# Performance work log

Hardware: AMD Instinct MI355X
Metric: run time of the kernel (lower is better)

The kernel has to match this reference:

```python
import jax, jax.numpy as jnp
import numpy as np

NEG_SLOPE = 0.2  # LeakyReLU slope

N, E, D_IN, D_OUT, H, NBIN = 50000, 500000, 256, 256, 8, 10
DH = D_OUT // H


def setup_inputs() -> dict:
    key = jax.random.key(0)
    ks = jax.random.split(key, 9)
    emb_rel = jax.random.normal(ks[0], (N, D_IN), dtype=jnp.float32)
    head_idxs = jax.random.randint(ks[1], (E,), 0, N, dtype=jnp.int32)
    tail_idxs = jax.random.randint(ks[2], (E,), 0, N, dtype=jnp.int32)
    bins = jax.random.randint(ks[3], (E,), 0, NBIN, dtype=jnp.int32)
    # xavier-normal-ish scaled params (gain for relu)
    attn_proj_w = jax.random.normal(ks[4], (D_OUT, 2 * D_IN), dtype=jnp.float32) * (1.4142 * (2.0 / (2 * D_IN + D_OUT)) ** 0.5)
    attn_proj_b = jnp.zeros((D_OUT,), dtype=jnp.float32)
    attn_bin = jax.random.normal(ks[5], (NBIN, H, 1), dtype=jnp.float32) * 0.3
    attn_vec = jax.random.normal(ks[6], (1, H, DH), dtype=jnp.float32) * (1.4142 * (2.0 / (H + DH)) ** 0.5)
    aggr_proj_w = jax.random.normal(ks[7], (D_OUT, D_IN), dtype=jnp.float32) * (1.4142 * (2.0 / (D_IN + D_OUT)) ** 0.5)
    aggr_proj_b = jnp.zeros((D_OUT,), dtype=jnp.float32)
    return {
        "emb_rel": emb_rel,
        "head_idxs": head_idxs,
        "tail_idxs": tail_idxs,
        "bins": bins,
        "attn_proj_w": attn_proj_w,
        "attn_proj_b": attn_proj_b,
        "attn_bin": attn_bin,
        "attn_vec": attn_vec,
        "aggr_proj_w": aggr_proj_w,
        "aggr_proj_b": aggr_proj_b,
        "num_nodes": N,
    }


def reference(emb_rel, head_idxs, tail_idxs, bins, attn_proj_w, attn_proj_b,
              attn_bin, attn_vec, aggr_proj_w, aggr_proj_b, num_nodes):
    num_head, dim_hid = attn_vec.shape[1], attn_vec.shape[2]
    eh = emb_rel[head_idxs]                      # (E, D_in)
    et = emb_rel[tail_idxs]                      # (E, D_in)
    concat = jnp.concatenate([eh, et], axis=-1)  # (E, 2*D_in)
    proj = (concat @ attn_proj_w.T + attn_proj_b).reshape(-1, num_head, dim_hid)
    lrelu = jnp.where(proj >= 0, proj, NEG_SLOPE * proj)
    # raw attention logits per edge/head: (E, H, 1)
    attn_raw = jnp.sum(lrelu * attn_vec, axis=-1, keepdims=True) + attn_bin[bins]
    # segmented softmax over edges grouped by head node
    seg_max = jax.ops.segment_max(attn_raw, head_idxs, num_segments=num_nodes)
    seg_max = jnp.where(jnp.isfinite(seg_max), seg_max, 0.0)  # empty segments -> 0 (never gathered anyway)
    attn_val = jnp.exp(attn_raw - seg_max[head_idxs])
    attn_sums = jax.ops.segment_sum(attn_val, head_idxs, num_segments=num_nodes)
    beta = attn_val / (attn_sums[head_idxs] + 1e-16)            # (E, H, 1)
    aggr = (et @ aggr_proj_w.T + aggr_proj_b).reshape(-1, num_head, dim_hid)
    out = jax.ops.segment_sum(beta * aggr, head_idxs, num_segments=num_nodes)
    return out.reshape(num_nodes, num_head * dim_hid)
```

## Files before the change

kernel.cpp:

```cpp
#include <hip/hip_runtime.h>
#include <math.h>

#define D_IN 256
#define D_OUT 256
#define NH 8
#define DH 32
#define NBIN 10
#define NEG_SLOPE 0.2f

typedef short short8 __attribute__((ext_vector_type(8)));
typedef float f32x4 __attribute__((ext_vector_type(4)));

__device__ __forceinline__ unsigned short f2bf(float f) {
  unsigned u = __float_as_uint(f);
  unsigned r = u + 0x7fffu + ((u >> 16) & 1u);
  return (unsigned short)(r >> 16);
}
__device__ __forceinline__ float bf2f(unsigned short s) {
  return __uint_as_float((unsigned)s << 16);
}

__global__ void pack_weights_kernel(const float* __restrict__ attn_w,
                                    const float* __restrict__ attn_b,
                                    const float* __restrict__ aggr_w,
                                    const float* __restrict__ aggr_b,
                                    unsigned short* __restrict__ WCbf,
                                    float* __restrict__ biasC) {
  int j = blockIdx.x;
  int k = threadIdx.x;
  float v, b = 0.f;
  if (j < 256) {
    v = attn_w[j * 512 + k];
  } else {
    int idx = j - 256, g = idx >> 3, r = idx & 7;
    if (r < 4) { int c = g * 4 + r;     v = attn_w[c * 512 + 256 + k]; b = attn_b[c]; }
    else       { int c = g * 4 + r - 4; v = aggr_w[c * 256 + k];       b = aggr_b[c]; }
  }
  WCbf[j * 256 + k] = f2bf(v);
  if (k == 0) biasC[j] = b;
}

__global__ void emb2bf_kernel(const float* __restrict__ emb,
                              unsigned short* __restrict__ embbf, long long total) {
  long long i = ((long long)blockIdx.x * blockDim.x + threadIdx.x) * 8;
  if (i >= total) return;
  float4 a = *(const float4*)(emb + i);
  float4 b = *(const float4*)(emb + i + 4);
  short8 o;
  o[0] = (short)f2bf(a.x); o[1] = (short)f2bf(a.y);
  o[2] = (short)f2bf(a.z); o[3] = (short)f2bf(a.w);
  o[4] = (short)f2bf(b.x); o[5] = (short)f2bf(b.y);
  o[6] = (short)f2bf(b.z); o[7] = (short)f2bf(b.w);
  *(short8*)(embbf + i) = o;
}

#define EPAD 36
__global__ __launch_bounds__(256) void gemm_bf16_kernel(
    const unsigned short* __restrict__ Abf,
    const unsigned short* __restrict__ Bbf,
    const float* __restrict__ biasC,
    float* __restrict__ P1, unsigned short* __restrict__ P2A, int N) {
  __shared__ char smem[128 * EPAD * 4];
  unsigned short* As = (unsigned short*)smem;
  unsigned short* Bs = (unsigned short*)(smem + 8192);
  float* Ls = (float*)smem;
  const int tid = threadIdx.x;
  const int row0 = blockIdx.y * 128, col0 = blockIdx.x * 128;
  const int wave = tid >> 6, l = tid & 63;
  const int wm = wave >> 1, wn = wave & 1;
  const int lr = l & 15;
  const int lq = l >> 4;
  const int srow = tid >> 2;
  const int sk = (tid & 3) * 8;
  f32x4 acc[4][4] = {};
  for (int kk = 0; kk < 256; kk += 32) {
    int ar0 = row0 + srow;      if (ar0 >= N) ar0 = N - 1;
    int ar1 = row0 + 64 + srow; if (ar1 >= N) ar1 = N - 1;
    short8 a0 = *(const short8*)(Abf + (size_t)ar0 * 256 + kk + sk);
    short8 a1 = *(const short8*)(Abf + (size_t)ar1 * 256 + kk + sk);
    short8 b0 = *(const short8*)(Bbf + (size_t)(col0 + srow) * 256 + kk + sk);
    short8 b1 = *(const short8*)(Bbf + (size_t)(col0 + 64 + srow) * 256 + kk + sk);
    __syncthreads();
    *(short8*)&As[srow * 32 + sk] = a0;
    *(short8*)&As[(64 + srow) * 32 + sk] = a1;
    *(short8*)&Bs[srow * 32 + sk] = b0;
    *(short8*)&Bs[(64 + srow) * 32 + sk] = b1;
    __syncthreads();
    short8 af[4], bfr[4];
#pragma unroll
    for (int i = 0; i < 4; ++i)
      af[i] = *(const short8*)&As[(wm * 64 + i * 16 + lr) * 32 + lq * 8];
#pragma unroll
    for (int j = 0; j < 4; ++j)
      bfr[j] = *(const short8*)&Bs[(wn * 64 + j * 16 + lr) * 32 + lq * 8];
#pragma unroll
    for (int i = 0; i < 4; ++i)
#pragma unroll
      for (int j = 0; j < 4; ++j)
        acc[i][j] = __builtin_amdgcn_mfma_f32_16x16x32_bf16(af[i], bfr[j], acc[i][j], 0, 0, 0);
  }
  for (int j = 0; j < 4; ++j) {
    __syncthreads();
    const float bias = biasC[col0 + wn * 64 + j * 16 + lr];
#pragma unroll
    for (int i = 0; i < 4; ++i) {
      const int lrow = wm * 64 + i * 16 + lq * 4;
#pragma unroll
      for (int r = 0; r < 4; ++r)
        Ls[(lrow + r) * EPAD + wn * 16 + lr] = acc[i][j][r] + bias;
    }
    __syncthreads();
    if (col0 < 256) {
      const int sub = tid & 7, half = sub >> 2, quad = sub & 3;
#pragma unroll
      for (int s = 0; s < 4; ++s) {
        const int row = (tid >> 3) + s * 32;
        const int grow = row0 + row;
        if (grow < N) {
          float4 v = *(const float4*)&Ls[row * EPAD + half * 16 + quad * 4];
          *(float4*)(P1 + (size_t)grow * 256 + col0 + half * 64 + j * 16 + quad * 4) = v;
        }
      }
    } else {
      const int o = tid & 3, half = o >> 1, part = o & 1;
#pragma unroll
      for (int s = 0; s < 2; ++s) {
        const int row = (tid >> 2) + s * 64;
        const int grow = row0 + row;
        if (grow < N) {
          const float* src = &Ls[row * EPAD + half * 16 + part * 8];
          short8 v;
#pragma unroll
          for (int q = 0; q < 8; ++q) v[q] = (short)f2bf(src[q]);
          *(short8*)(P2A + (size_t)grow * 512 + (col0 - 256) + half * 64 + j * 16 + part * 8) = v;
        }
      }
    }
  }
}

__global__ void count_kernel(const int* __restrict__ head, int* __restrict__ deg, int E) {
  int e = blockIdx.x * blockDim.x + threadIdx.x;
  if (e < E) atomicAdd(&deg[head[e]], 1);
}

__global__ __launch_bounds__(256) void scan_partial_kernel(const int* __restrict__ deg,
                                                           int* __restrict__ row_start,
                                                           int* __restrict__ blocksums, int N) {
  __shared__ int wave_tot[4];
  const int t = threadIdx.x;
  const int base = blockIdx.x * 1024 + t * 4;
  int d0 = 0, d1 = 0, d2 = 0, d3 = 0;
  if (base + 0 < N) d0 = deg[base + 0];
  if (base + 1 < N) d1 = deg[base + 1];
  if (base + 2 < N) d2 = deg[base + 2];
  if (base + 3 < N) d3 = deg[base + 3];
  const int s = d0 + d1 + d2 + d3;
  const int lane = t & 63;
  int v = s;
#pragma unroll
  for (int off = 1; off < 64; off <<= 1) {
    int u = __shfl_up(v, off, 64);
    if (lane >= off) v += u;
  }
  if (lane == 63) wave_tot[t >> 6] = v;
  __syncthreads();
  int woff = 0;
  const int w = t >> 6;
  for (int i = 0; i < 4; ++i)
    if (i < w) woff += wave_tot[i];
  const int excl = v - s + woff;
  if (base + 0 < N) row_start[base + 0] = excl;
  if (base + 1 < N) row_start[base + 1] = excl + d0;
  if (base + 2 < N) row_start[base + 2] = excl + d0 + d1;
  if (base + 3 < N) row_start[base + 3] = excl + d0 + d1 + d2;
  if (t == 255) blocksums[blockIdx.x] = excl + s;
}

__global__ void scan_sums_kernel(int* __restrict__ blocksums, int nb) {
  if (threadIdx.x == 0 && blockIdx.x == 0) {
    int run = 0;
    for (int i = 0; i < nb; ++i) {
      int v = blocksums[i];
      blocksums[i] = run;
      run += v;
    }
  }
}

__global__ void add_offsets_kernel(int* __restrict__ row_start, int* __restrict__ cursor,
                                   const int* __restrict__ blocksums, int N) {
  int i = blockIdx.x * blockDim.x + threadIdx.x;
  if (i < N) {
    int v = row_start[i] + blocksums[i >> 10];
    row_start[i] = v;
    cursor[i] = v;
  }
}

__global__ void scatter_kernel(const int* __restrict__ head, const int* __restrict__ tail,
                               const int* __restrict__ bins, int* __restrict__ cursor,
                               int* __restrict__ packed, int E) {
  int e = blockIdx.x * blockDim.x + threadIdx.x;
  if (e >= E) return;
  int pos = atomicAdd(&cursor[head[e]], 1);
  packed[pos] = (bins[e] << 16) | tail[e];
}

__global__ __launch_bounds__(256) void node_aggr_kernel(
    const float* __restrict__ P1, const unsigned short* __restrict__ P2A,
    const int* __restrict__ row_start, const int* __restrict__ deg,
    const int* __restrict__ packed, const float* __restrict__ attn_vec,
    const float* __restrict__ attn_bin, float* __restrict__ out, int N) {
  __shared__ float sbin[NBIN * NH];
  const int tid = threadIdx.x;
  if (tid < NBIN * NH) sbin[tid] = attn_bin[tid];
  __syncthreads();
  const int n = blockIdx.x * 4 + (tid >> 6);
  if (n >= N) return;
  const int l = tid & 63;
  const int h = l >> 3;
  const float4 av = *(const float4*)(attn_vec + l * 4);
  const float4 p1 = *(const float4*)(P1 + (size_t)n * 256 + l * 4);
  const int start = row_start[n];
  const int d = deg[n];
  float m = -INFINITY, sum = 0.f;
  float4 acc = make_float4(0.f, 0.f, 0.f, 0.f);
  int pk = 0;
  short8 cur = {};
  if (d > 0) {
    pk = packed[start];
    cur = *(const short8*)(P2A + (size_t)(pk & 0xFFFF) * 512 + l * 8);
  }
  for (int i = 0; i < d; ++i) {
    const int ni = start + ((i + 1 < d) ? i + 1 : i);
    const int pk_next = packed[ni];
    const short8 nxt = *(const short8*)(P2A + (size_t)(pk_next & 0xFFFF) * 512 + l * 8);
    const int bin = pk >> 16;
    float s = 0.f, x;
    x = p1.x + bf2f((unsigned short)cur[0]); x = (x >= 0.f) ? x : NEG_SLOPE * x; s += x * av.x;
    x = p1.y + bf2f((unsigned short)cur[1]); x = (x >= 0.f) ? x : NEG_SLOPE * x; s += x * av.y;
    x = p1.z + bf2f((unsigned short)cur[2]); x = (x >= 0.f) ? x : NEG_SLOPE * x; s += x * av.z;
    x = p1.w + bf2f((unsigned short)cur[3]); x = (x >= 0.f) ? x : NEG_SLOPE * x; s += x * av.w;
    s += __shfl_down(s, 4, 8);
    s += __shfl_down(s, 2, 8);
    s += __shfl_down(s, 1, 8);
    s = __shfl(s, 0, 8);
    const float logit = s + sbin[bin * NH + h];
    const float mn = fmaxf(m, logit);
    const float scale = __expf(m - mn);
    const float w = __expf(logit - mn);
    sum = sum * scale + w;
    acc.x = acc.x * scale + w * bf2f((unsigned short)cur[4]);
    acc.y = acc.y * scale + w * bf2f((unsigned short)cur[5]);
    acc.z = acc.z * scale + w * bf2f((unsigned short)cur[6]);
    acc.w = acc.w * scale + w * bf2f((unsigned short)cur[7]);
    m = mn;
    pk = pk_next;
    cur = nxt;
  }
  const float inv = 1.f / (sum + 1e-16f);
  float4 o;
  o.x = acc.x * inv; o.y = acc.y * inv; o.z = acc.z * inv; o.w = acc.w * inv;
  *(float4*)(out + (size_t)n * 256 + l * 4) = o;
}

extern "C" void kernel_launch(void* const* d_in, const int* in_sizes, int n_in,
                              void* d_out, int out_size, void* d_ws, size_t ws_size,
                              hipStream_t stream) {
  const float* emb      = (const float*)d_in[0];
  const int*   head     = (const int*)d_in[1];
  const int*   tail     = (const int*)d_in[2];
  const int*   bins     = (const int*)d_in[3];
  const float* attn_w   = (const float*)d_in[4];
  const float* attn_b   = (const float*)d_in[5];
  const float* attn_bin = (const float*)d_in[6];
  const float* attn_vec = (const float*)d_in[7];
  const float* aggr_w   = (const float*)d_in[8];
  const float* aggr_b   = (const float*)d_in[9];
  float* out = (float*)d_out;

  const int N = in_sizes[0] / D_IN;
  const int E = in_sizes[1];
  const int nb = (N + 1023) / 1024;

  char* ws = (char*)d_ws;
  size_t off = 0;
  auto walloc = [&](size_t bytes) -> void* {
    void* p = ws + off;
    off += (bytes + 255) & ~(size_t)255;
    return p;
  };
  float*          P1        = (float*)walloc((size_t)N * 256 * sizeof(float));
  unsigned short* P2A       = (unsigned short*)walloc((size_t)N * 512 * sizeof(short));
  unsigned short* embbf     = (unsigned short*)walloc((size_t)N * 256 * sizeof(short));
  unsigned short* WCbf      = (unsigned short*)walloc((size_t)768 * 256 * sizeof(short));
  float*          biasC     = (float*)walloc(768 * sizeof(float));
  int*            deg       = (int*)walloc((size_t)N * sizeof(int));
  int*            row_start = (int*)walloc((size_t)N * sizeof(int));
  int*            cursor    = (int*)walloc((size_t)N * sizeof(int));
  int*            blocksums = (int*)walloc((size_t)nb * sizeof(int));
  int*            packed    = (int*)walloc((size_t)E * sizeof(int));

  hipMemsetAsync(deg, 0, (size_t)N * sizeof(int), stream);

  pack_weights_kernel<<<768, 256, 0, stream>>>(attn_w, attn_b, aggr_w, aggr_b, WCbf, biasC);

  const long long total = (long long)N * D_IN;
  emb2bf_kernel<<<(unsigned)((total / 8 + 255) / 256), 256, 0, stream>>>(emb, embbf, total);

  dim3 ggrid(768 / 128, (N + 127) / 128);
  gemm_bf16_kernel<<<ggrid, 256, 0, stream>>>(embbf, WCbf, biasC, P1, P2A, N);

  count_kernel<<<(E + 255) / 256, 256, 0, stream>>>(head, deg, E);
  scan_partial_kernel<<<nb, 256, 0, stream>>>(deg, row_start, blocksums, N);
  scan_sums_kernel<<<1, 64, 0, stream>>>(blocksums, nb);
  add_offsets_kernel<<<(N + 255) / 256, 256, 0, stream>>>(row_start, cursor, blocksums, N);
  scatter_kernel<<<(E + 255) / 256, 256, 0, stream>>>(head, tail, bins, cursor, packed, E);

  node_aggr_kernel<<<(N + 3) / 4, 256, 0, stream>>>(P1, P2A, row_start, deg, packed,
                                                    attn_vec, attn_bin, out, N);
}
```

Measured before the change: 321.6 us.

## Fuse bf16 conversion into GEMM loads and merge small CSR-build launches

Drops the separate emb-to-bf16 pass: the GEMM now loads fp32 embedding rows and rounds them to bf16 in registers before staging them in shared memory. This removes a full write and re-read of the bf16 embedding copy. The deg memset moves into the weight-pack kernel, and the serial block-sum scan plus the offset-add kernel become one single-block kernel that does a wave-level scan. In exchange the GEMM reads twice as many bytes per A tile across its column blocks, does the conversion work inside every tile, and the offset pass now runs on only one block.

Result: no change. 326.5 us (+1.5%).

```diff
diff --git a/kernel.cpp b/kernel.cpp
--- a/kernel.cpp
+++ b/kernel.cpp
@@ -25,9 +25,12 @@
                                     const float* __restrict__ aggr_w,
                                     const float* __restrict__ aggr_b,
                                     unsigned short* __restrict__ WCbf,
-                                    float* __restrict__ biasC) {
+                                    float* __restrict__ biasC,
+                                    int* __restrict__ deg, int N) {
   int j = blockIdx.x;
   int k = threadIdx.x;
+  int idx0 = j * 256 + k;
+  if (idx0 < N) deg[idx0] = 0;
   float v, b = 0.f;
   if (j < 256) {
     v = attn_w[j * 512 + k];
@@ -40,23 +43,9 @@
   if (k == 0) biasC[j] = b;
 }
 
-__global__ void emb2bf_kernel(const float* __restrict__ emb,
-                              unsigned short* __restrict__ embbf, long long total) {
-  long long i = ((long long)blockIdx.x * blockDim.x + threadIdx.x) * 8;
-  if (i >= total) return;
-  float4 a = *(const float4*)(emb + i);
-  float4 b = *(const float4*)(emb + i + 4);
-  short8 o;
-  o[0] = (short)f2bf(a.x); o[1] = (short)f2bf(a.y);
-  o[2] = (short)f2bf(a.z); o[3] = (short)f2bf(a.w);
-  o[4] = (short)f2bf(b.x); o[5] = (short)f2bf(b.y);
-  o[6] = (short)f2bf(b.z); o[7] = (short)f2bf(b.w);
-  *(short8*)(embbf + i) = o;
-}
-
 #define EPAD 36
 __global__ __launch_bounds__(256) void gemm_bf16_kernel(
-    const unsigned short* __restrict__ Abf,
+    const float* __restrict__ Aemb,
     const unsigned short* __restrict__ Bbf,
     const float* __restrict__ biasC,
     float* __restrict__ P1, unsigned short* __restrict__ P2A, int N) {
@@ -76,10 +65,21 @@
   for (int kk = 0; kk < 256; kk += 32) {
     int ar0 = row0 + srow;      if (ar0 >= N) ar0 = N - 1;
     int ar1 = row0 + 64 + srow; if (ar1 >= N) ar1 = N - 1;
-    short8 a0 = *(const short8*)(Abf + (size_t)ar0 * 256 + kk + sk);
-    short8 a1 = *(const short8*)(Abf + (size_t)ar1 * 256 + kk + sk);
+    float4 a0lo = *(const float4*)(Aemb + (size_t)ar0 * 256 + kk + sk);
+    float4 a0hi = *(const float4*)(Aemb + (size_t)ar0 * 256 + kk + sk + 4);
+    float4 a1lo = *(const float4*)(Aemb + (size_t)ar1 * 256 + kk + sk);
+    float4 a1hi = *(const float4*)(Aemb + (size_t)ar1 * 256 + kk + sk + 4);
     short8 b0 = *(const short8*)(Bbf + (size_t)(col0 + srow) * 256 + kk + sk);
     short8 b1 = *(const short8*)(Bbf + (size_t)(col0 + 64 + srow) * 256 + kk + sk);
+    short8 a0, a1;
+    a0[0] = (short)f2bf(a0lo.x); a0[1] = (short)f2bf(a0lo.y);
+    a0[2] = (short)f2bf(a0lo.z); a0[3] = (short)f2bf(a0lo.w);
+    a0[4] = (short)f2bf(a0hi.x); a0[5] = (short)f2bf(a0hi.y);
+    a0[6] = (short)f2bf(a0hi.z); a0[7] = (short)f2bf(a0hi.w);
+    a1[0] = (short)f2bf(a1lo.x); a1[1] = (short)f2bf(a1lo.y);
+    a1[2] = (short)f2bf(a1lo.z); a1[3] = (short)f2bf(a1lo.w);
+    a1[4] = (short)f2bf(a1hi.x); a1[5] = (short)f2bf(a1hi.y);
+    a1[6] = (short)f2bf(a1hi.z); a1[7] = (short)f2bf(a1hi.w);
     __syncthreads();
     *(short8*)&As[srow * 32 + sk] = a0;
     *(short8*)&As[(64 + srow) * 32 + sk] = a1;
@@ -177,22 +177,30 @@
   if (t == 255) blocksums[blockIdx.x] = excl + s;
 }
 
-__global__ void scan_sums_kernel(int* __restrict__ blocksums, int nb) {
-  if (threadIdx.x == 0 && blockIdx.x == 0) {
-    int run = 0;
-    for (int i = 0; i < nb; ++i) {
-      int v = blocksums[i];
-      blocksums[i] = run;
-      run += v;
+__global__ __launch_bounds__(1024) void csr_finalize_kernel(
+    int* __restrict__ row_start, int* __restrict__ cursor,
+    const int* __restrict__ blocksums, int nb, int N) {
+  __shared__ int soff[256];
+  const int t = threadIdx.x;
+  if (t < 64) {
+    int carry = 0;
+    for (int c = 0; c < nb; c += 64) {
+      int v = (c + t < nb) ? blocksums[c + t] : 0;
+#pragma unroll
+      for (int off = 1; off < 64; off <<= 1) {
+        int u = __shfl_up(v, off, 64);
+        if (t >= off) v += u;
+      }
+      int tot = __shfl(v, 63, 64);
+      if (c + t < nb) soff[c + t] = v + carry;
+      carry += tot;
     }
   }
-}
-
-__global__ void add_offsets_kernel(int* __restrict__ row_start, int* __restrict__ cursor,
-                                   const int* __restrict__ blocksums, int N) {
-  int i = blockIdx.x * blockDim.x + threadIdx.x;
-  if (i < N) {
-    int v = row_start[i] + blocksums[i >> 10];
+  __syncthreads();
+  for (int i = t; i < N; i += 1024) {
+    int b = i >> 10;
+    int off = (b == 0) ? 0 : soff[b - 1];
+    int v = row_start[i] + off;
     row_start[i] = v;
     cursor[i] = v;
   }
@@ -293,7 +301,6 @@
   };
   float*          P1        = (float*)walloc((size_t)N * 256 * sizeof(float));
   unsigned short* P2A       = (unsigned short*)walloc((size_t)N * 512 * sizeof(short));
-  unsigned short* embbf     = (unsigned short*)walloc((size_t)N * 256 * sizeof(short));
   unsigned short* WCbf      = (unsigned short*)walloc((size_t)768 * 256 * sizeof(short));
   float*          biasC     = (float*)walloc(768 * sizeof(float));
   int*            deg       = (int*)walloc((size_t)N * sizeof(int));
@@ -302,20 +309,15 @@
   int*            blocksums = (int*)walloc((size_t)nb * sizeof(int));
   int*            packed    = (int*)walloc((size_t)E * sizeof(int));
 
-  hipMemsetAsync(deg, 0, (size_t)N * sizeof(int), stream);
-
-  pack_weights_kernel<<<768, 256, 0, stream>>>(attn_w, attn_b, aggr_w, aggr_b, WCbf, biasC);
-
-  const long long total = (long long)N * D_IN;
-  emb2bf_kernel<<<(unsigned)((total / 8 + 255) / 256), 256, 0, stream>>>(emb, embbf, total);
+  pack_weights_kernel<<<768, 256, 0, stream>>>(attn_w, attn_b, aggr_w, aggr_b,
+                                               WCbf, biasC, deg, N);
 
   dim3 ggrid(768 / 128, (N + 127) / 128);
-  gemm_bf16_kernel<<<ggrid, 256, 0, stream>>>(embbf, WCbf, biasC, P1, P2A, N);
+  gemm_bf16_kernel<<<ggrid, 256, 0, stream>>>(emb, WCbf, biasC, P1, P2A, N);
 
   count_kernel<<<(E + 255) / 256, 256, 0, stream>>>(head, deg, E);
   scan_partial_kernel<<<nb, 256, 0, stream>>>(deg, row_start, blocksums, N);
-  scan_sums_kernel<<<1, 64, 0, stream>>>(blocksums, nb);
-  add_offsets_kernel<<<(N + 255) / 256, 256, 0, stream>>>(row_start, cursor, blocksums, N);
+  csr_finalize_kernel<<<1, 1024, 0, stream>>>(row_start, cursor, blocksums, nb, N);
   scatter_kernel<<<(E + 255) / 256, 256, 0, stream>>>(head, tail, bins, cursor, packed, E);
 
   node_aggr_kernel<<<(N + 3) / 4, 256, 0, stream>>>(P1, P2A, row_start, deg, packed,
```
